# Optimization experiments

Hardware: AMD Instinct MI355X
Metric: run time of the kernel (lower is better)

The kernel has to match this reference:

```python
import jax, jax.numpy as jnp
import numpy as np

D_K = 128
NEG_BIG = 1e32  # matches torch's -1e+32 additive mask (finite in fp32)


def setup_inputs() -> dict:
    key = jax.random.key(0)
    kq, kk, kv, kqp, kkp = jax.random.split(key, 5)
    B, M, N, d_k, d_v = 8, 2048, 2048, D_K, 128
    return {
        "queries": jax.random.normal(kq, (B, M, d_k), dtype=jnp.float32),
        "keys": jax.random.normal(kk, (B, N, d_k), dtype=jnp.float32),
        "values": jax.random.normal(kv, (B, N, d_v), dtype=jnp.float32),
        "q_pres": jax.random.randint(kqp, (B, M), 0, 2, dtype=jnp.int32),
        "k_pres": jax.random.randint(kkp, (B, N), 0, 2, dtype=jnp.int32),
    }


def reference(queries, keys, values, q_pres, k_pres):
    # routing: [B, M, N] = Q K^T with multiplicative presence masking
    routing = jnp.einsum("bmd,bnd->bmn", queries, keys)
    qp = q_pres.astype(jnp.float32)  # [B, M]
    kp = k_pres.astype(jnp.float32)  # [B, N]
    routing = routing * qp[:, :, None]
    routing = routing * kp[:, None, :]
    # additive -1e32 mask for absent keys, then scaled softmax over N
    routing = routing - (1.0 - kp[:, None, :]) * NEG_BIG
    routing = jax.nn.softmax(routing / np.sqrt(D_K).astype(np.float32), axis=-1)
    return jnp.einsum("bmn,bnv->bmv", routing, values)
```

## Files before the change

kernel.cpp:

```cpp
#include <hip/hip_runtime.h>
#include <cstddef>
#include <cstdint>

#define SEQ_M 2048
#define SEQ_N 2048
#define DKV 128
#define BN 64
#define NCH 4
#define CHKEYS (SEQ_N / NCH)
#define NKT 32
#define MT2 16
#define MTB 8
#define NREC (NCH * 8 * MT2)

typedef _Float16 f16x8 __attribute__((ext_vector_type(8)));
typedef _Float16 f16x4 __attribute__((ext_vector_type(4)));
typedef float f32x4 __attribute__((ext_vector_type(4)));

#if defined(__has_builtin)
#if __has_builtin(__builtin_amdgcn_exp2f)
#define EXP2F(x) __builtin_amdgcn_exp2f(x)
#else
#define EXP2F(x) exp2f(x)
#endif
#else
#define EXP2F(x) exp2f(x)
#endif

#define SM_SCALE 0.12751745f
#define BIG_NEG 1.2751745e31f
#define MSHIFT 8.0f

#define KH_OFF 0
#define VH_OFF (256 * 8192)
#define P16_OFF (2 * 256 * 8192)
#define L_BYTE_OFF ((size_t)(P16_OFF + (size_t)NREC * 16384) * 2)
#define WS_NEED (L_BYTE_OFF + (size_t)NREC * 128 * 4)

#define AS1 __attribute__((address_space(1)))
#define AS3 __attribute__((address_space(3)))

__device__ __forceinline__ void copy16(const void* g, void* lds_base,
                                       void* lds_lane) {
#if defined(__has_builtin) && __has_builtin(__builtin_amdgcn_global_load_lds)
  __builtin_amdgcn_global_load_lds((const AS1 void*)g, (AS3 void*)lds_base, 16,
                                   0, 0);
  (void)lds_lane;
#else
  *(f16x8*)lds_lane = *(const f16x8*)g;
#endif
}

__global__ __launch_bounds__(256) void prep(const float* __restrict__ Kg,
                                            const float* __restrict__ Vg,
                                            _Float16* __restrict__ Kh,
                                            _Float16* __restrict__ Vh) {
  const int T = blockIdx.x >> 2;
  const int kind = blockIdx.x & 1;
  const int half = (blockIdx.x >> 1) & 1;
  const int b = T >> 5, nt = T & 31;
  const int t = threadIdx.x;
  if (kind == 0) {
    const float* Kb = Kg + ((size_t)b * SEQ_N + nt * 64) * DKV;
    _Float16* Kt_ = Kh + (size_t)T * 8192;
#pragma unroll
    for (int i = 0; i < 2; ++i) {
      const int idx = half * 512 + i * 256 + t;
      const int c = idx & 15, key = idx >> 4;
      const float* src = Kb + key * DKV + c * 8;
      const float4 a0 = *(const float4*)src;
      const float4 a1 = *(const float4*)(src + 4);
      f16x8 h;
      h[0] = (_Float16)a0.x; h[1] = (_Float16)a0.y;
      h[2] = (_Float16)a0.z; h[3] = (_Float16)a0.w;
      h[4] = (_Float16)a1.x; h[5] = (_Float16)a1.y;
      h[6] = (_Float16)a1.z; h[7] = (_Float16)a1.w;
      *(f16x8*)&Kt_[c * 512 + key * 8] = h;
    }
  } else {
    const float* Vb = Vg + ((size_t)b * SEQ_N + nt * 64) * DKV;
    _Float16* Vt_ = Vh + (size_t)T * 8192;
#pragma unroll
    for (int i = 0; i < 2; ++i) {
      const int idx = half * 512 + i * 256 + t;
      const int vcol = idx & 127, g = idx >> 7;
      f16x8 h;
#pragma unroll
      for (int j = 0; j < 8; ++j)
        h[j] = (_Float16)Vb[(size_t)(g * 8 + j) * DKV + vcol];
      *(f16x8*)&Vt_[vcol * 64 + ((g ^ (vcol & 7)) * 8)] = h;
    }
  }
}

__global__ __launch_bounds__(512, 2) void attn_core6(
    const _Float16* __restrict__ Kh, const _Float16* __restrict__ Vh,
    const float* __restrict__ Qg, const int* __restrict__ QPg,
    const int* __restrict__ KPg, _Float16* __restrict__ P16,
    float* __restrict__ Lw) {
  __shared__ _Float16 smem[4 * 8192 + 8 * 2304];
  _Float16* const Kt0 = smem;
  _Float16* const Vt0 = smem + 8192;
  _Float16* const Kt1 = smem + 16384;
  _Float16* const Vt1 = smem + 24576;

  const int tid = threadIdx.x;
  const int w = tid >> 6;
  const int lane = tid & 63;
  const int q16 = lane & 15;
  const int quad = lane >> 4;
  _Float16* const Pl = smem + 32768 + w * 2304;

  const int b = blockIdx.x & 7;
  const int rest = blockIdx.x >> 3;
  const int mt = rest & 7;
  const int chk = rest >> 3;

  auto STAGE = [&](int nt, _Float16* ktDst, _Float16* vtDst) {
    const char* gsrc =
        (w < 4) ? (const char*)(Kh + (size_t)(b * NKT + nt) * 8192) +
                      (w & 3) * 4096
                : (const char*)(Vh + (size_t)(b * NKT + nt) * 8192) +
                      (w & 3) * 4096;
    char* ldst = (w < 4) ? (char*)ktDst + (w & 3) * 4096
                         : (char*)vtDst + (w & 3) * 4096;
#pragma unroll
    for (int r = 0; r < 4; ++r)
      copy16(gsrc + r * 1024 + lane * 16, ldst + r * 1024,
             ldst + r * 1024 + lane * 16);
  };

  STAGE(chk * 8 + 0, Kt0, Vt0);

  const int qrowA = mt * 256 + w * 32 + q16;
  const float* qptrA = Qg + ((size_t)b * SEQ_M + qrowA) * DKV;
  const float* qptrB = qptrA + 16 * DKV;
  const float qsA = QPg[b * SEQ_M + qrowA] ? 1.0f : 0.0f;
  const float qsB = QPg[b * SEQ_M + qrowA + 16] ? 1.0f : 0.0f;
  f16x8 qfA[4], qfB[4];
#pragma unroll
  for (int kc = 0; kc < 4; ++kc) {
    const float4 a0 = *(const float4*)(qptrA + kc * 32 + quad * 8);
    const float4 a1 = *(const float4*)(qptrA + kc * 32 + quad * 8 + 4);
    f16x8 h;
    h[0] = (_Float16)(a0.x * qsA); h[1] = (_Float16)(a0.y * qsA);
    h[2] = (_Float16)(a0.z * qsA); h[3] = (_Float16)(a0.w * qsA);
    h[4] = (_Float16)(a1.x * qsA); h[5] = (_Float16)(a1.y * qsA);
    h[6] = (_Float16)(a1.z * qsA); h[7] = (_Float16)(a1.w * qsA);
    qfA[kc] = h;
    const float4 b0 = *(const float4*)(qptrB + kc * 32 + quad * 8);
    const float4 b1 = *(const float4*)(qptrB + kc * 32 + quad * 8 + 4);
    f16x8 g;
    g[0] = (_Float16)(b0.x * qsB); g[1] = (_Float16)(b0.y * qsB);
    g[2] = (_Float16)(b0.z * qsB); g[3] = (_Float16)(b0.w * qsB);
    g[4] = (_Float16)(b1.x * qsB); g[5] = (_Float16)(b1.y * qsB);
    g[6] = (_Float16)(b1.z * qsB); g[7] = (_Float16)(b1.w * qsB);
    qfB[kc] = g;
  }

  unsigned long long km[8];
#pragma unroll
  for (int ti = 0; ti < 8; ++ti)
    km[ti] = __ballot(
        KPg[(size_t)b * SEQ_N + (size_t)(chk * 8 + ti) * 64 + lane] != 0);

  f32x4 oA[8], oB[8];
#pragma unroll
  for (int vt = 0; vt < 8; ++vt) {
    oA[vt] = (f32x4){0.f, 0.f, 0.f, 0.f};
    oB[vt] = (f32x4){0.f, 0.f, 0.f, 0.f};
  }
  float plA = 0.f, plB = 0.f;

  auto COMPUTE = [&](const _Float16* KtC, const _Float16* VtC,
                     const unsigned long long kmask) {
    f32x4 stA[4], stB[4];
#pragma unroll
    for (int t = 0; t < 4; ++t) {
      stA[t] = (f32x4){0.f, 0.f, 0.f, 0.f};
      stB[t] = (f32x4){0.f, 0.f, 0.f, 0.f};
    }
#pragma unroll
    for (int kc = 0; kc < 4; ++kc) {
      const f16x8 qvA = qfA[kc];
      const f16x8 qvB = qfB[kc];
#pragma unroll
      for (int t = 0; t < 4; ++t) {
        const f16x8 kf =
            *(const f16x8*)&KtC[((kc * 4 + quad) * 64 + t * 16 + q16) * 8];
        stA[t] =
            __builtin_amdgcn_mfma_f32_16x16x32_f16(kf, qvA, stA[t], 0, 0, 0);
        stB[t] =
            __builtin_amdgcn_mfma_f32_16x16x32_f16(kf, qvB, stB[t], 0, 0, 0);
      }
    }

    float pA[16], pB[16];
#pragma unroll
    for (int t = 0; t < 4; ++t)
#pragma unroll
      for (int r = 0; r < 4; ++r) {
        const int key = t * 16 + quad * 4 + r;
        const bool on = (kmask >> key) & 1ull;
        const float eA = EXP2F(stA[t][r] * SM_SCALE - MSHIFT);
        const float eB = EXP2F(stB[t][r] * SM_SCALE - MSHIFT);
        const float vA = on ? eA : 0.f;
        const float vB = on ? eB : 0.f;
        pA[t * 4 + r] = vA; plA += vA;
        pB[t * 4 + r] = vB; plB += vB;
      }

#pragma unroll
    for (int t = 0; t < 4; ++t) {
      f16x4 pwA, pwB;
#pragma unroll
      for (int r = 0; r < 4; ++r) {
        pwA[r] = (_Float16)pA[t * 4 + r];
        pwB[r] = (_Float16)pB[t * 4 + r];
      }
      *(f16x4*)&Pl[q16 * 72 + t * 16 + quad * 4] = pwA;
      *(f16x4*)&Pl[(16 + q16) * 72 + t * 16 + quad * 4] = pwB;
    }
    const f16x8 pfA0 = *(const f16x8*)&Pl[q16 * 72 + quad * 8];
    const f16x8 pfA1 = *(const f16x8*)&Pl[q16 * 72 + 32 + quad * 8];
    const f16x8 pfB0 = *(const f16x8*)&Pl[(16 + q16) * 72 + quad * 8];
    const f16x8 pfB1 = *(const f16x8*)&Pl[(16 + q16) * 72 + 32 + quad * 8];

#pragma unroll
    for (int vt = 0; vt < 8; ++vt) {
      const int vcol = vt * 16 + q16;
      const f16x8 v0 =
          *(const f16x8*)&VtC[vcol * 64 + ((quad ^ (vcol & 7)) * 8)];
      const f16x8 v1 =
          *(const f16x8*)&VtC[vcol * 64 + (((quad + 4) ^ (vcol & 7)) * 8)];
      oA[vt] =
          __builtin_amdgcn_mfma_f32_16x16x32_f16(pfA0, v0, oA[vt], 0, 0, 0);
      oA[vt] =
          __builtin_amdgcn_mfma_f32_16x16x32_f16(pfA1, v1, oA[vt], 0, 0, 0);
      oB[vt] =
          __builtin_amdgcn_mfma_f32_16x16x32_f16(pfB0, v0, oB[vt], 0, 0, 0);
      oB[vt] =
          __builtin_amdgcn_mfma_f32_16x16x32_f16(pfB1, v1, oB[vt], 0, 0, 0);
    }
  };

  __syncthreads();

#pragma unroll
  for (int ti = 0; ti < 8; ++ti) {
    _Float16* const KtC = (ti & 1) ? Kt1 : Kt0;
    _Float16* const VtC = (ti & 1) ? Vt1 : Vt0;
    _Float16* const KtN = (ti & 1) ? Kt0 : Kt1;
    _Float16* const VtN = (ti & 1) ? Vt0 : Vt1;
    if (ti + 1 < 8) STAGE(chk * 8 + ti + 1, KtN, VtN);
    COMPUTE(KtC, VtC, km[ti]);
    __syncthreads();
  }

  plA += __shfl_xor(plA, 16); plA += __shfl_xor(plA, 32);
  plB += __shfl_xor(plB, 16); plB += __shfl_xor(plB, 32);
  float liA[4], liB[4];
#pragma unroll
  for (int r = 0; r < 4; ++r) {
    liA[r] = 1.0f / __shfl(plA, quad * 4 + r);
    liB[r] = 1.0f / __shfl(plB, quad * 4 + r);
  }
  const int rec = (chk * 8 + b) * MT2 + (mt * 2 + (w >> 2));
  _Float16* obA = P16 + (size_t)rec * 16384 + (size_t)((w & 3) * 32) * 128;
  _Float16* obB = obA + 16 * 128;
#pragma unroll
  for (int vt = 0; vt < 8; ++vt)
#pragma unroll
    for (int r = 0; r < 4; ++r) {
      obA[(quad * 4 + r) * 128 + vt * 16 + q16] =
          (_Float16)(oA[vt][r] * liA[r]);
      obB[(quad * 4 + r) * 128 + vt * 16 + q16] =
          (_Float16)(oB[vt][r] * liB[r]);
    }
  if (quad == 0) {
    float* lr = Lw + (size_t)rec * 128;
    lr[(w & 3) * 32 + q16] = plA;
    lr[(w & 3) * 32 + 16 + q16] = plB;
  }
}

__global__ __launch_bounds__(256) void attn_combine4(
    const _Float16* __restrict__ P16, const float* __restrict__ Lw,
    float* __restrict__ Og) {
  const int t = threadIdx.x;
  const int b = blockIdx.x & 7;
  const int rest = blockIdx.x >> 3;
  const int mt = rest & 15;
  const int ch = rest >> 4;
  __shared__ float lsh[NCH][128];
#pragma unroll
  for (int i = 0; i < 2; ++i) {
    const int idx = i * 256 + t;
    const int c = idx >> 7, row = idx & 127;
    lsh[c][row] = Lw[(size_t)((c * 8 + b) * MT2 + mt) * 128 + row];
  }
  __syncthreads();
  const int colh = ch * 64 + (t & 15) * 4;
  const int rg = t >> 4;
  const _Float16* recO[NCH];
#pragma unroll
  for (int c = 0; c < NCH; ++c)
    recO[c] = P16 + (size_t)((c * 8 + b) * MT2 + mt) * 16384;
  float* outb = Og + ((size_t)b * SEQ_M + mt * 128) * DKV;
#pragma unroll
  for (int rr = 0; rr < 8; ++rr) {
    const int row = rr * 16 + rg;
    float lt = 0.f;
#pragma unroll
    for (int c = 0; c < NCH; ++c) lt += lsh[c][row];
    const float inv = 1.0f / lt;
    f32x4 acc = (f32x4){0.f, 0.f, 0.f, 0.f};
#pragma unroll
    for (int c = 0; c < NCH; ++c) {
      const float wc = lsh[c][row];
      const f16x4 v = *(const f16x4*)(recO[c] + (size_t)row * 128 + colh);
      acc[0] += wc * (float)v[0]; acc[1] += wc * (float)v[1];
      acc[2] += wc * (float)v[2]; acc[3] += wc * (float)v[3];
    }
    f32x4 r;
    r[0] = acc[0] * inv; r[1] = acc[1] * inv;
    r[2] = acc[2] * inv; r[3] = acc[3] * inv;
    *(f32x4*)(outb + (size_t)row * DKV + colh) = r;
  }
}

__global__ __launch_bounds__(256) void attn_fallback(
    const float* __restrict__ Qg, const float* __restrict__ Kg,
    const float* __restrict__ Vg, const int* __restrict__ QPg,
    const int* __restrict__ KPg, float* __restrict__ Og) {
  __shared__ _Float16 smem[16 * 65 * 8 + 128 * 72];
  _Float16* const Kt = smem;
  _Float16* const Vt = smem + 16 * 65 * 8;
  const int tid = threadIdx.x;
  const int w = tid >> 6;
  const int lane = tid & 63;
  const int q16 = lane & 15;
  const int quad = lane >> 4;
  _Float16* const Pl = smem + w * (16 * 72);
  const int b = blockIdx.x & 7;
  const int mb = (blockIdx.x >> 3) * 64;
  const int qrow = mb + w * 16 + q16;
  const float* qptr = Qg + ((size_t)b * SEQ_M + qrow) * DKV;
  const float qs = QPg[b * SEQ_M + qrow] ? 1.0f : 0.0f;
  f16x8 qf[4];
#pragma unroll
  for (int kc = 0; kc < 4; ++kc) {
    const float4 a0 = *(const float4*)(qptr + kc * 32 + quad * 8);
    const float4 a1 = *(const float4*)(qptr + kc * 32 + quad * 8 + 4);
    f16x8 h;
    h[0] = (_Float16)(a0.x * qs); h[1] = (_Float16)(a0.y * qs);
    h[2] = (_Float16)(a0.z * qs); h[3] = (_Float16)(a0.w * qs);
    h[4] = (_Float16)(a1.x * qs); h[5] = (_Float16)(a1.y * qs);
    h[6] = (_Float16)(a1.z * qs); h[7] = (_Float16)(a1.w * qs);
    qf[kc] = h;
  }
  f32x4 o[8];
#pragma unroll
  for (int vt = 0; vt < 8; ++vt) o[vt] = (f32x4){0.f, 0.f, 0.f, 0.f};
  float m_run = -3.0e38f, l_run = 0.f;
  const int kn = tid >> 2, ks = (tid & 3) * 32;
  const int vg = tid >> 3, vk = (tid & 7) * 8;
  for (int n0 = 0; n0 < SEQ_N; n0 += BN) {
    __syncthreads();
    {
      const float* kp_ = Kg + ((size_t)b * SEQ_N + n0 + kn) * DKV + ks;
#pragma unroll
      for (int c2 = 0; c2 < 4; ++c2) {
        const float4 a0 = *(const float4*)(kp_ + c2 * 8);
        const float4 a1 = *(const float4*)(kp_ + c2 * 8 + 4);
        f16x8 h;
        h[0] = (_Float16)a0.x; h[1] = (_Float16)a0.y;
        h[2] = (_Float16)a0.z; h[3] = (_Float16)a0.w;
        h[4] = (_Float16)a1.x; h[5] = (_Float16)a1.y;
        h[6] = (_Float16)a1.z; h[7] = (_Float16)a1.w;
        *(f16x8*)&Kt[(((ks >> 3) + c2) * 65 + kn) * 8] = h;
      }
    }
    {
      const float* vp0 = Vg + ((size_t)b * SEQ_N + n0 + vk) * DKV + vg * 4;
      float4 vv[8];
#pragma unroll
      for (int j = 0; j < 8; ++j) vv[j] = *(const float4*)(vp0 + (size_t)j * DKV);
#pragma unroll
      for (int i = 0; i < 4; ++i) {
        f16x8 h;
#pragma unroll
        for (int j = 0; j < 8; ++j) h[j] = (_Float16)(((const float*)&vv[j])[i]);
        *(f16x8*)&Vt[(vg * 4 + i) * 72 + vk] = h;
      }
    }
    const unsigned long long kmask =
        __ballot(KPg[(size_t)b * SEQ_N + n0 + lane] != 0);
    __syncthreads();
    f32x4 st[4];
#pragma unroll
    for (int t = 0; t < 4; ++t) st[t] = (f32x4){0.f, 0.f, 0.f, 0.f};
#pragma unroll
    for (int kc = 0; kc < 4; ++kc) {
      const f16x8 qv = qf[kc];
#pragma unroll
      for (int t = 0; t < 4; ++t) {
        const f16x8 kf =
            *(const f16x8*)&Kt[((kc * 4 + quad) * 65 + t * 16 + q16) * 8];
        st[t] = __builtin_amdgcn_mfma_f32_16x16x32_f16(kf, qv, st[t], 0, 0, 0);
      }
    }
    float s2[16];
    float mx = -3.0e38f;
#pragma unroll
    for (int t = 0; t < 4; ++t)
#pragma unroll
      for (int r = 0; r < 4; ++r) {
        const int key = t * 16 + quad * 4 + r;
        const float v =
            ((kmask >> key) & 1ull) ? st[t][r] * SM_SCALE : -BIG_NEG;
        s2[t * 4 + r] = v;
        mx = fmaxf(mx, v);
      }
    mx = fmaxf(mx, __shfl_xor(mx, 16));
    mx = fmaxf(mx, __shfl_xor(mx, 32));
    const float mnew = fmaxf(m_run, mx);
    const float alpha = EXP2F(m_run - mnew);
    m_run = mnew;
    float p[16];
    float psum = 0.f;
#pragma unroll
    for (int i = 0; i < 16; ++i) {
      p[i] = EXP2F(s2[i] - mnew);
      psum += p[i];
    }
    psum += __shfl_xor(psum, 16);
    psum += __shfl_xor(psum, 32);
    l_run = l_run * alpha + psum;
    float arow[4];
#pragma unroll
    for (int r = 0; r < 4; ++r) arow[r] = __shfl(alpha, quad * 4 + r);
#pragma unroll
    for (int vt = 0; vt < 8; ++vt) {
      o[vt][0] *= arow[0]; o[vt][1] *= arow[1];
      o[vt][2] *= arow[2]; o[vt][3] *= arow[3];
    }
    __syncthreads();
#pragma unroll
    for (int t = 0; t < 4; ++t) {
      f16x4 pw;
      pw[0] = (_Float16)p[t * 4 + 0];
      pw[1] = (_Float16)p[t * 4 + 1];
      pw[2] = (_Float16)p[t * 4 + 2];
      pw[3] = (_Float16)p[t * 4 + 3];
      *(f16x4*)&Pl[q16 * 72 + t * 16 + quad * 4] = pw;
    }
    const f16x8 pf0 = *(const f16x8*)&Pl[q16 * 72 + quad * 8];
    const f16x8 pf1 = *(const f16x8*)&Pl[q16 * 72 + 32 + quad * 8];
#pragma unroll
    for (int vt = 0; vt < 8; ++vt) {
      const f16x8 v0 = *(const f16x8*)&Vt[(vt * 16 + q16) * 72 + quad * 8];
      o[vt] = __builtin_amdgcn_mfma_f32_16x16x32_f16(pf0, v0, o[vt], 0, 0, 0);
      const f16x8 v1 = *(const f16x8*)&Vt[(vt * 16 + q16) * 72 + 32 + quad * 8];
      o[vt] = __builtin_amdgcn_mfma_f32_16x16x32_f16(pf1, v1, o[vt], 0, 0, 0);
    }
  }
  float linv[4];
#pragma unroll
  for (int r = 0; r < 4; ++r) linv[r] = 1.0f / __shfl(l_run, quad * 4 + r);
  float* obase = Og + ((size_t)b * SEQ_M + mb + w * 16) * DKV;
#pragma unroll
  for (int vt = 0; vt < 8; ++vt)
#pragma unroll
    for (int r = 0; r < 4; ++r)
      obase[(size_t)(quad * 4 + r) * DKV + vt * 16 + q16] = o[vt][r] * linv[r];
}

extern "C" void kernel_launch(void* const* d_in, const int* in_sizes, int n_in,
                              void* d_out, int out_size, void* d_ws,
                              size_t ws_size, hipStream_t stream) {
  const float* Q = (const float*)d_in[0];
  const float* K = (const float*)d_in[1];
  const float* V = (const float*)d_in[2];
  const int* QP = (const int*)d_in[3];
  const int* KP = (const int*)d_in[4];
  float* O = (float*)d_out;
  if (ws_size >= WS_NEED) {
    _Float16* wsh = (_Float16*)d_ws;
    _Float16* Kh = wsh + KH_OFF;
    _Float16* Vh = wsh + VH_OFF;
    _Float16* P16 = wsh + P16_OFF;
    float* Lw = (float*)((char*)d_ws + L_BYTE_OFF);
    prep<<<dim3(1024), dim3(256), 0, stream>>>(K, V, Kh, Vh);
    attn_core6<<<dim3(8 * MTB * NCH), dim3(512), 0, stream>>>(
        Kh, Vh, Q, QP, KP, P16, Lw);
    attn_combine4<<<dim3(8 * MT2 * 2), dim3(256), 0, stream>>>(P16, Lw, O);
  } else {
    attn_fallback<<<dim3(8 * 32), dim3(256), 0, stream>>>(Q, K, V, QP, KP, O);
  }
}
```

Measured before the change: 111.2 us.

## Switch attention core to 32x32x16 MFMA with permlane P transpose

Rewrites the core attention kernel to use 32x32x16 f16 MFMA tiles instead of 16x16x32. The P matrix is moved from the QK^T output layout into the PV operand layout with permlane32_swap in registers, so the per-wave LDS round trip for P goes away. Blocks shrink from 512 to 256 threads, each handling 128 query rows, which doubles the grid size and cuts LDS per block. In exchange, each block does twice the K/V staging per query row, and the larger MFMA accumulators add register pressure.

```diff
diff --git a/kernel.cpp b/kernel.cpp
--- a/kernel.cpp
+++ b/kernel.cpp
@@ -10,12 +10,15 @@
 #define CHKEYS (SEQ_N / NCH)
 #define NKT 32
 #define MT2 16
-#define MTB 8
 #define NREC (NCH * 8 * MT2)
 
 typedef _Float16 f16x8 __attribute__((ext_vector_type(8)));
 typedef _Float16 f16x4 __attribute__((ext_vector_type(4)));
+typedef _Float16 f16x2 __attribute__((ext_vector_type(2)));
 typedef float f32x4 __attribute__((ext_vector_type(4)));
+typedef float f32x16 __attribute__((ext_vector_type(16)));
+typedef unsigned int u32x2 __attribute__((ext_vector_type(2)));
+typedef unsigned int u32x4 __attribute__((ext_vector_type(4)));
 
 #if defined(__has_builtin)
 #if __has_builtin(__builtin_amdgcn_exp2f)
@@ -25,6 +28,12 @@
 #endif
 #else
 #define EXP2F(x) exp2f(x)
+#endif
+
+#if defined(__has_builtin)
+#if __has_builtin(__builtin_amdgcn_permlane32_swap)
+#define HAVE_PLSWAP 1
+#endif
 #endif
 
 #define SM_SCALE 0.12751745f
@@ -48,6 +57,21 @@
   (void)lds_lane;
 #else
   *(f16x8*)lds_lane = *(const f16x8*)g;
+#endif
+}
+
+__device__ __forceinline__ void pswap(unsigned int a, unsigned int b, int hi,
+                                      unsigned int& o0, unsigned int& o1) {
+#if defined(HAVE_PLSWAP)
+  u32x2 r = __builtin_amdgcn_permlane32_swap(a, b, false, false);
+  o0 = r[0];
+  o1 = r[1];
+  (void)hi;
+#else
+  const unsigned int as = __shfl_xor(a, 32);
+  const unsigned int bs = __shfl_xor(b, 32);
+  o0 = hi ? bs : a;
+  o1 = hi ? b : as;
 #endif
 }
 
@@ -93,12 +117,12 @@
   }
 }
 
-__global__ __launch_bounds__(512, 2) void attn_core6(
+__global__ __launch_bounds__(256, 2) void attn_core7(
     const _Float16* __restrict__ Kh, const _Float16* __restrict__ Vh,
     const float* __restrict__ Qg, const int* __restrict__ QPg,
     const int* __restrict__ KPg, _Float16* __restrict__ P16,
     float* __restrict__ Lw) {
-  __shared__ _Float16 smem[4 * 8192 + 8 * 2304];
+  __shared__ _Float16 smem[4 * 8192];
   _Float16* const Kt0 = smem;
   _Float16* const Vt0 = smem + 8192;
   _Float16* const Kt1 = smem + 16384;
@@ -107,55 +131,43 @@
   const int tid = threadIdx.x;
   const int w = tid >> 6;
   const int lane = tid & 63;
-  const int q16 = lane & 15;
-  const int quad = lane >> 4;
-  _Float16* const Pl = smem + 32768 + w * 2304;
+  const int lam = lane & 31;
+  const int hi = lane >> 5;
 
   const int b = blockIdx.x & 7;
   const int rest = blockIdx.x >> 3;
-  const int mt = rest & 7;
-  const int chk = rest >> 3;
-
-  auto STAGE = [&](int nt, _Float16* ktDst, _Float16* vtDst) {
+  const int mt = rest & 15;
+  const int chk = rest >> 4;
+
+  auto STAGE = [&](int nt, _Float16* ktD, _Float16* vtD) {
     const char* gsrc =
-        (w < 4) ? (const char*)(Kh + (size_t)(b * NKT + nt) * 8192) +
-                      (w & 3) * 4096
+        (w < 2) ? (const char*)(Kh + (size_t)(b * NKT + nt) * 8192) + w * 8192
                 : (const char*)(Vh + (size_t)(b * NKT + nt) * 8192) +
-                      (w & 3) * 4096;
-    char* ldst = (w < 4) ? (char*)ktDst + (w & 3) * 4096
-                         : (char*)vtDst + (w & 3) * 4096;
-#pragma unroll
-    for (int r = 0; r < 4; ++r)
+                      (w - 2) * 8192;
+    char* ldst = (w < 2) ? (char*)ktD + w * 8192 : (char*)vtD + (w - 2) * 8192;
+#pragma unroll
+    for (int r = 0; r < 8; ++r)
       copy16(gsrc + r * 1024 + lane * 16, ldst + r * 1024,
              ldst + r * 1024 + lane * 16);
   };
 
   STAGE(chk * 8 + 0, Kt0, Vt0);
 
-  const int qrowA = mt * 256 + w * 32 + q16;
-  const float* qptrA = Qg + ((size_t)b * SEQ_M + qrowA) * DKV;
-  const float* qptrB = qptrA + 16 * DKV;
-  const float qsA = QPg[b * SEQ_M + qrowA] ? 1.0f : 0.0f;
-  const float qsB = QPg[b * SEQ_M + qrowA + 16] ? 1.0f : 0.0f;
-  f16x8 qfA[4], qfB[4];
-#pragma unroll
-  for (int kc = 0; kc < 4; ++kc) {
-    const float4 a0 = *(const float4*)(qptrA + kc * 32 + quad * 8);
-    const float4 a1 = *(const float4*)(qptrA + kc * 32 + quad * 8 + 4);
+  const int qrow = mt * 128 + w * 32 + lam;
+  const float* qptr = Qg + ((size_t)b * SEQ_M + qrow) * DKV;
+  const float qs = QPg[b * SEQ_M + qrow] ? 1.0f : 0.0f;
+  f16x8 qf[8];
+#pragma unroll
+  for (int ks16 = 0; ks16 < 8; ++ks16) {
+    const float* src = qptr + ks16 * 16 + hi * 8;
+    const float4 a0 = *(const float4*)src;
+    const float4 a1 = *(const float4*)(src + 4);
     f16x8 h;
-    h[0] = (_Float16)(a0.x * qsA); h[1] = (_Float16)(a0.y * qsA);
-    h[2] = (_Float16)(a0.z * qsA); h[3] = (_Float16)(a0.w * qsA);
-    h[4] = (_Float16)(a1.x * qsA); h[5] = (_Float16)(a1.y * qsA);
-    h[6] = (_Float16)(a1.z * qsA); h[7] = (_Float16)(a1.w * qsA);
-    qfA[kc] = h;
-    const float4 b0 = *(const float4*)(qptrB + kc * 32 + quad * 8);
-    const float4 b1 = *(const float4*)(qptrB + kc * 32 + quad * 8 + 4);
-    f16x8 g;
-    g[0] = (_Float16)(b0.x * qsB); g[1] = (_Float16)(b0.y * qsB);
-    g[2] = (_Float16)(b0.z * qsB); g[3] = (_Float16)(b0.w * qsB);
-    g[4] = (_Float16)(b1.x * qsB); g[5] = (_Float16)(b1.y * qsB);
-    g[6] = (_Float16)(b1.z * qsB); g[7] = (_Float16)(b1.w * qsB);
-    qfB[kc] = g;
+    h[0] = (_Float16)(a0.x * qs); h[1] = (_Float16)(a0.y * qs);
+    h[2] = (_Float16)(a0.z * qs); h[3] = (_Float16)(a0.w * qs);
+    h[4] = (_Float16)(a1.x * qs); h[5] = (_Float16)(a1.y * qs);
+    h[6] = (_Float16)(a1.z * qs); h[7] = (_Float16)(a1.w * qs);
+    qf[ks16] = h;
   }
 
   unsigned long long km[8];
@@ -164,85 +176,12 @@
     km[ti] = __ballot(
         KPg[(size_t)b * SEQ_N + (size_t)(chk * 8 + ti) * 64 + lane] != 0);
 
-  f32x4 oA[8], oB[8];
-#pragma unroll
-  for (int vt = 0; vt < 8; ++vt) {
-    oA[vt] = (f32x4){0.f, 0.f, 0.f, 0.f};
-    oB[vt] = (f32x4){0.f, 0.f, 0.f, 0.f};
-  }
-  float plA = 0.f, plB = 0.f;
-
-  auto COMPUTE = [&](const _Float16* KtC, const _Float16* VtC,
-                     const unsigned long long kmask) {
-    f32x4 stA[4], stB[4];
-#pragma unroll
-    for (int t = 0; t < 4; ++t) {
-      stA[t] = (f32x4){0.f, 0.f, 0.f, 0.f};
-      stB[t] = (f32x4){0.f, 0.f, 0.f, 0.f};
-    }
-#pragma unroll
-    for (int kc = 0; kc < 4; ++kc) {
-      const f16x8 qvA = qfA[kc];
-      const f16x8 qvB = qfB[kc];
-#pragma unroll
-      for (int t = 0; t < 4; ++t) {
-        const f16x8 kf =
-            *(const f16x8*)&KtC[((kc * 4 + quad) * 64 + t * 16 + q16) * 8];
-        stA[t] =
-            __builtin_amdgcn_mfma_f32_16x16x32_f16(kf, qvA, stA[t], 0, 0, 0);
-        stB[t] =
-            __builtin_amdgcn_mfma_f32_16x16x32_f16(kf, qvB, stB[t], 0, 0, 0);
-      }
-    }
-
-    float pA[16], pB[16];
-#pragma unroll
-    for (int t = 0; t < 4; ++t)
-#pragma unroll
-      for (int r = 0; r < 4; ++r) {
-        const int key = t * 16 + quad * 4 + r;
-        const bool on = (kmask >> key) & 1ull;
-        const float eA = EXP2F(stA[t][r] * SM_SCALE - MSHIFT);
-        const float eB = EXP2F(stB[t][r] * SM_SCALE - MSHIFT);
-        const float vA = on ? eA : 0.f;
-        const float vB = on ? eB : 0.f;
-        pA[t * 4 + r] = vA; plA += vA;
-        pB[t * 4 + r] = vB; plB += vB;
-      }
-
-#pragma unroll
-    for (int t = 0; t < 4; ++t) {
-      f16x4 pwA, pwB;
-#pragma unroll
-      for (int r = 0; r < 4; ++r) {
-        pwA[r] = (_Float16)pA[t * 4 + r];
-        pwB[r] = (_Float16)pB[t * 4 + r];
-      }
-      *(f16x4*)&Pl[q16 * 72 + t * 16 + quad * 4] = pwA;
-      *(f16x4*)&Pl[(16 + q16) * 72 + t * 16 + quad * 4] = pwB;
-    }
-    const f16x8 pfA0 = *(const f16x8*)&Pl[q16 * 72 + quad * 8];
-    const f16x8 pfA1 = *(const f16x8*)&Pl[q16 * 72 + 32 + quad * 8];
-    const f16x8 pfB0 = *(const f16x8*)&Pl[(16 + q16) * 72 + quad * 8];
-    const f16x8 pfB1 = *(const f16x8*)&Pl[(16 + q16) * 72 + 32 + quad * 8];
-
-#pragma unroll
-    for (int vt = 0; vt < 8; ++vt) {
-      const int vcol = vt * 16 + q16;
-      const f16x8 v0 =
-          *(const f16x8*)&VtC[vcol * 64 + ((quad ^ (vcol & 7)) * 8)];
-      const f16x8 v1 =
-          *(const f16x8*)&VtC[vcol * 64 + (((quad + 4) ^ (vcol & 7)) * 8)];
-      oA[vt] =
-          __builtin_amdgcn_mfma_f32_16x16x32_f16(pfA0, v0, oA[vt], 0, 0, 0);
-      oA[vt] =
-          __builtin_amdgcn_mfma_f32_16x16x32_f16(pfA1, v1, oA[vt], 0, 0, 0);
-      oB[vt] =
-          __builtin_amdgcn_mfma_f32_16x16x32_f16(pfB0, v0, oB[vt], 0, 0, 0);
-      oB[vt] =
-          __builtin_amdgcn_mfma_f32_16x16x32_f16(pfB1, v1, oB[vt], 0, 0, 0);
-    }
-  };
+  f32x16 o[4];
+#pragma unroll
+  for (int vt = 0; vt < 4; ++vt)
+#pragma unroll
+    for (int r = 0; r < 16; ++r) o[vt][r] = 0.f;
+  float pl = 0.f;
 
   __syncthreads();
 
@@ -253,35 +192,82 @@
     _Float16* const KtN = (ti & 1) ? Kt0 : Kt1;
     _Float16* const VtN = (ti & 1) ? Vt0 : Vt1;
     if (ti + 1 < 8) STAGE(chk * 8 + ti + 1, KtN, VtN);
-    COMPUTE(KtC, VtC, km[ti]);
+    const unsigned long long kmask = km[ti];
+
+    f32x16 st0, st1;
+#pragma unroll
+    for (int r = 0; r < 16; ++r) { st0[r] = 0.f; st1[r] = 0.f; }
+#pragma unroll
+    for (int ks16 = 0; ks16 < 8; ++ks16) {
+      const f16x8 qv = qf[ks16];
+      const int c = ks16 * 2 + hi;
+      const f16x8 k0 = *(const f16x8*)&KtC[c * 512 + (0 * 32 + lam) * 8];
+      const f16x8 k1 = *(const f16x8*)&KtC[c * 512 + (1 * 32 + lam) * 8];
+      st0 = __builtin_amdgcn_mfma_f32_32x32x16_f16(k0, qv, st0, 0, 0, 0);
+      st1 = __builtin_amdgcn_mfma_f32_32x32x16_f16(k1, qv, st1, 0, 0, 0);
+    }
+
+    float p[2][16];
+#pragma unroll
+    for (int kt = 0; kt < 2; ++kt)
+#pragma unroll
+      for (int reg = 0; reg < 16; ++reg) {
+        const int keybase = kt * 32 + (reg & 3) + 8 * (reg >> 2);
+        const bool b0 = (kmask >> keybase) & 1ull;
+        const bool b4 = (kmask >> (keybase + 4)) & 1ull;
+        const float s = (kt ? st1[reg] : st0[reg]) * SM_SCALE - MSHIFT;
+        const float e = EXP2F(s);
+        const float v = (hi ? b4 : b0) ? e : 0.f;
+        p[kt][reg] = v;
+        pl += v;
+      }
+
+    unsigned int pk[2][8];
+#pragma unroll
+    for (int kt = 0; kt < 2; ++kt)
+#pragma unroll
+      for (int m = 0; m < 8; ++m) {
+        f16x2 hh;
+        hh[0] = (_Float16)p[kt][2 * m];
+        hh[1] = (_Float16)p[kt][2 * m + 1];
+        pk[kt][m] = __builtin_bit_cast(unsigned int, hh);
+      }
+
+#pragma unroll
+    for (int ks = 0; ks < 4; ++ks) {
+      const int kt = ks >> 1, k16 = ks & 1;
+      unsigned int f0, f2, f1, f3;
+      pswap(pk[kt][4 * k16 + 0], pk[kt][4 * k16 + 2], hi, f0, f2);
+      pswap(pk[kt][4 * k16 + 1], pk[kt][4 * k16 + 3], hi, f1, f3);
+      const u32x4 pa4 = {f0, f1, f2, f3};
+      const f16x8 paf = __builtin_bit_cast(f16x8, pa4);
+      const int g = ks * 2 + hi;
+#pragma unroll
+      for (int vt = 0; vt < 4; ++vt) {
+        const int vcol = vt * 32 + lam;
+        const f16x8 vf = *(const f16x8*)&VtC[vcol * 64 + ((g ^ (vcol & 7)) * 8)];
+        o[vt] = __builtin_amdgcn_mfma_f32_32x32x16_f16(paf, vf, o[vt], 0, 0, 0);
+      }
+    }
     __syncthreads();
   }
 
-  plA += __shfl_xor(plA, 16); plA += __shfl_xor(plA, 32);
-  plB += __shfl_xor(plB, 16); plB += __shfl_xor(plB, 32);
-  float liA[4], liB[4];
-#pragma unroll
-  for (int r = 0; r < 4; ++r) {
-    liA[r] = 1.0f / __shfl(plA, quad * 4 + r);
-    liB[r] = 1.0f / __shfl(plB, quad * 4 + r);
-  }
-  const int rec = (chk * 8 + b) * MT2 + (mt * 2 + (w >> 2));
-  _Float16* obA = P16 + (size_t)rec * 16384 + (size_t)((w & 3) * 32) * 128;
-  _Float16* obB = obA + 16 * 128;
-#pragma unroll
-  for (int vt = 0; vt < 8; ++vt)
-#pragma unroll
-    for (int r = 0; r < 4; ++r) {
-      obA[(quad * 4 + r) * 128 + vt * 16 + q16] =
-          (_Float16)(oA[vt][r] * liA[r]);
-      obB[(quad * 4 + r) * 128 + vt * 16 + q16] =
-          (_Float16)(oB[vt][r] * liB[r]);
-    }
-  if (quad == 0) {
-    float* lr = Lw + (size_t)rec * 128;
-    lr[(w & 3) * 32 + q16] = plA;
-    lr[(w & 3) * 32 + 16 + q16] = plB;
-  }
+  pl += __shfl_xor(pl, 32);
+  const int rec = (chk * 8 + b) * MT2 + mt;
+  if (lane < 32) Lw[(size_t)rec * 128 + w * 32 + lam] = pl;
+  float li[16];
+#pragma unroll
+  for (int reg = 0; reg < 16; ++reg)
+    li[reg] = 1.0f / __shfl(pl, (reg & 3) + 8 * (reg >> 2) + 4 * hi);
+
+  _Float16* ob = P16 + (size_t)rec * 16384 + (size_t)(w * 32) * 128;
+#pragma unroll
+  for (int vt = 0; vt < 4; ++vt)
+#pragma unroll
+    for (int reg = 0; reg < 16; ++reg) {
+      const int q = (reg & 3) + 8 * (reg >> 2) + 4 * hi;
+      ob[q * 128 + vt * 32 + lam] = (_Float16)(o[vt][reg] * li[reg]);
+    }
 }
 
 __global__ __launch_bounds__(256) void attn_combine4(
@@ -492,7 +478,7 @@
     _Float16* P16 = wsh + P16_OFF;
     float* Lw = (float*)((char*)d_ws + L_BYTE_OFF);
     prep<<<dim3(1024), dim3(256), 0, stream>>>(K, V, Kh, Vh);
-    attn_core6<<<dim3(8 * MTB * NCH), dim3(512), 0, stream>>>(
+    attn_core7<<<dim3(8 * MT2 * NCH), dim3(256), 0, stream>>>(
         Kh, Vh, Q, QP, KP, P16, Lw);
     attn_combine4<<<dim3(8 * MT2 * 2), dim3(256), 0, stream>>>(P16, Lw, O);
   } else {
```

After: 111.1 us. No clear change (-0.1%).
